# Performance work log

Hardware: AMD Instinct MI355X
Metric: run time of the kernel (lower is better)

## Reference

```python
import jax, jax.numpy as jnp
import numpy as np

B, E, F, H, C = 2048, 16, 512, 1024, 512
TOP_K = 4
TEMP = 1.0


def setup_inputs() -> dict:
    key = jax.random.key(0)
    ks = jax.random.split(key, 5)
    h = jax.random.normal(ks[0], (B, F), jnp.float32)
    # Router posterior params (xavier-ish mu, logvar init at -7 as in torch code)
    W_mu = jax.random.normal(ks[1], (E, F), jnp.float32) * (1.0 / np.sqrt(F))
    W_logvar = jnp.full((E, F), -7.0, jnp.float32)
    b_mu = jnp.zeros((E,), jnp.float32)
    b_logvar = jnp.full((E,), -7.0, jnp.float32)
    # Expert MLP params: layer1 [F->H] relu, layer2 [H->C]
    W1 = jax.random.normal(ks[2], (E, F, H), jnp.float32) * (1.0 / np.sqrt(F))
    b1 = jnp.zeros((E, H), jnp.float32)
    W2 = jax.random.normal(ks[3], (E, H, C), jnp.float32) * (1.0 / np.sqrt(H))
    b2 = jnp.zeros((E, C), jnp.float32)
    return {"h": h, "W_mu": W_mu, "b_mu": b_mu, "W_logvar": W_logvar,
            "b_logvar": b_logvar, "W1": W1, "b1": b1, "W2": W2, "b2": b2}


def reference(h, W_mu, b_mu, W_logvar, b_logvar, W1, b1, W2, b2):
    # Bayesian router moments: mu = h @ W_mu^T + b_mu ; var = (h*h) @ exp(W_logvar)^T + exp(b_logvar)
    mu_m = h @ W_mu.T + b_mu                                   # [B,E]
    var_m = (h * h) @ jnp.exp(W_logvar).T + jnp.exp(b_logvar)  # [B,E]
    var_m = jnp.maximum(var_m, 1e-12)
    # Logistic-normal shrink: tilde = mu / sqrt(1 + (pi/8) var)
    tilde_m = mu_m / jnp.sqrt(1.0 + (jnp.pi / 8.0) * var_m)
    gate_probs = jax.nn.softmax(tilde_m / TEMP, axis=-1)       # [B,E]
    # Strict top-k by gate_scores (tilde_m), renormalize probs within top-k
    topk_scores, topk_idx = jax.lax.top_k(tilde_m, TOP_K)      # [B,k]
    topk_w = jnp.take_along_axis(gate_probs, topk_idx, axis=1) # [B,k]
    topk_w = topk_w / jnp.maximum(topk_w.sum(axis=1, keepdims=True), 1e-12)
    # Dense combine weights: w[b,e] = sum of renormalized top-k weights of token b for expert e
    Bsz = h.shape[0]
    w = jnp.zeros((Bsz, E), h.dtype).at[jnp.arange(Bsz)[:, None], topk_idx].add(topk_w)
    # Expert MLPs (grouped GEMM form); tokens not routed to expert e get weight 0
    a = jax.nn.relu(jnp.einsum('bf,efh->beh', h, W1) + b1)     # [B,E,H]
    y = jnp.einsum('beh,ehc->bec', a, W2) + b2                 # [B,E,C]
    combined = jnp.einsum('be,bec->bc', w, y)                  # [B,C]
    return combined
```

## Files before the change

kernel.cpp:

```cpp
#include <hip/hip_runtime.h>
#include <hip/hip_bf16.h>

typedef __attribute__((ext_vector_type(8))) short bf16x8;
typedef __attribute__((ext_vector_type(4))) float f32x4;

#define NTOK   2048
#define NEXP   16
#define NF     512
#define NH     1024
#define NCOUT  512
#define NPAIR  8192

__device__ __forceinline__ void gload16_lds(const __hip_bfloat16* g, const __hip_bfloat16* l) {
  __builtin_amdgcn_global_load_lds((const __attribute__((address_space(1))) void*)g,
                                   (__attribute__((address_space(3))) void*)l, 16, 0, 0);
}

__global__ __launch_bounds__(256) void router_kernel(
    const float* __restrict__ h, const float* __restrict__ W_mu,
    const float* __restrict__ b_mu, const float* __restrict__ W_logvar,
    const float* __restrict__ b_logvar,
    int* __restrict__ topk_idx, float* __restrict__ topk_w,
    __hip_bfloat16* __restrict__ hb)
{
  __shared__ __align__(16) float hs[NF], hs2[NF];
  __shared__ float smu[NEXP], svar[NEXP];
  const int b = blockIdx.x, tid = threadIdx.x;
  for (int i = tid; i < NF; i += 256) {
    float v = h[(size_t)b * NF + i];
    hs[i] = v; hs2[i] = v * v;
    hb[(size_t)b * NF + i] = __float2bfloat16(v);
  }
  __syncthreads();
  const int e = tid >> 4, l = tid & 15;
  float mu = 0.f, var = 0.f;
  const float4* wm4 = (const float4*)(W_mu + e * NF);
  const float4* wv4 = (const float4*)(W_logvar + e * NF);
  const float4* h4  = (const float4*)hs;
  const float4* h24 = (const float4*)hs2;
#pragma unroll
  for (int j = 0; j < NF / 64; ++j) {
    int i4 = l + j * 16;
    float4 a = h4[i4],  wa = wm4[i4];
    float4 c = h24[i4], wc = wv4[i4];
    mu  += a.x * wa.x + a.y * wa.y + a.z * wa.z + a.w * wa.w;
    var += c.x * __expf(wc.x) + c.y * __expf(wc.y) + c.z * __expf(wc.z) + c.w * __expf(wc.w);
  }
#pragma unroll
  for (int o = 1; o < 16; o <<= 1) { mu += __shfl_xor(mu, o); var += __shfl_xor(var, o); }
  if (l == 0) { smu[e] = mu + b_mu[e]; svar[e] = var + __expf(b_logvar[e]); }
  __syncthreads();
  if (tid < 64) {
    float val = -1e30f;
    if (tid < NEXP) {
      float v = fmaxf(svar[tid], 1e-12f);
      val = smu[tid] / sqrtf(1.0f + 0.39269908169872414f * v);
    }
    float mx = 0.f, wsum = 0.f;
    int i0, i1, i2, i3; float p0, p1, p2, p3;
#define TOPK_ROUND(ii, pp, FIRST)                                          \
    {                                                                      \
      float m = val;                                                       \
      m = fmaxf(m, __shfl_xor(m, 1));  m = fmaxf(m, __shfl_xor(m, 2));     \
      m = fmaxf(m, __shfl_xor(m, 4));  m = fmaxf(m, __shfl_xor(m, 8));     \
      m = fmaxf(m, __shfl_xor(m, 16)); m = fmaxf(m, __shfl_xor(m, 32));    \
      unsigned long long bm = __ballot(val == m);                          \
      int bi = (int)__builtin_ctzll(bm);                                   \
      if (FIRST) mx = m;                                                   \
      pp = expf(m - mx); wsum += pp; ii = bi;                              \
      if (tid == bi) val = -1e30f;                                         \
    }
    TOPK_ROUND(i0, p0, 1)
    TOPK_ROUND(i1, p1, 0)
    TOPK_ROUND(i2, p2, 0)
    TOPK_ROUND(i3, p3, 0)
#undef TOPK_ROUND
    if (tid == 0) {
      float inv = 1.0f / fmaxf(wsum, 1e-12f);
      topk_idx[b * 4 + 0] = i0; topk_w[b * 4 + 0] = p0 * inv;
      topk_idx[b * 4 + 1] = i1; topk_w[b * 4 + 1] = p1 * inv;
      topk_idx[b * 4 + 2] = i2; topk_w[b * 4 + 2] = p2 * inv;
      topk_idx[b * 4 + 3] = i3; topk_w[b * 4 + 3] = p3 * inv;
    }
  }
}

__global__ __launch_bounds__(1024) void route_finish_kernel(
    const int* __restrict__ topk_idx,
    int* __restrict__ counts, int* __restrict__ offsets,
    int* __restrict__ token_of_row, int* __restrict__ pair_row)
{
  __shared__ int cnt[128][16];
  __shared__ int choff[128][2];
  __shared__ int tot[16];
  __shared__ int soff[16];
  const int tid = threadIdx.x;
  const int wv = tid >> 6, ln = tid & 63;
  const int e0 = blockIdx.x * 2;
  int mye[8], myrank[8];
#pragma unroll
  for (int r = 0; r < 8; ++r) {
    const int chunk = r * 16 + wv;
    const int t = chunk * 64 + ln;
    const int e = topk_idx[t];
    mye[r] = e;
    unsigned long long mymask = 0;
#pragma unroll
    for (int ee = 0; ee < 16; ++ee) {
      unsigned long long bmask = __ballot(e == ee);
      if (ln == 0) cnt[chunk][ee] = __popcll(bmask);
      if (e == ee) mymask = bmask;
    }
    myrank[r] = __popcll(mymask & ((1ull << ln) - 1ull));
  }
  __syncthreads();
  if (tid < 16) {
    int run = 0;
    for (int c = 0; c < 128; ++c) run += cnt[c][tid];
    tot[tid] = run;
    if (blockIdx.x == 0) counts[tid] = run;
  }
  if (tid >= 32 && tid < 34) {
    const int e = e0 + (tid - 32);
    int run = 0;
    for (int c = 0; c < 128; ++c) { choff[c][tid - 32] = run; run += cnt[c][e]; }
  }
  __syncthreads();
  if (tid == 0) {
    int run = 0;
    for (int e2 = 0; e2 < NEXP; ++e2) {
      soff[e2] = run;
      if (blockIdx.x == 0) offsets[e2] = run;
      run += tot[e2];
    }
  }
  __syncthreads();
#pragma unroll
  for (int r = 0; r < 8; ++r) {
    const int e = mye[r];
    if (e == e0 || e == e0 + 1) {
      const int chunk = r * 16 + wv;
      const int t = chunk * 64 + ln;
      const int pos = soff[e] + choff[chunk][e - e0] + myrank[r];
      token_of_row[pos] = t >> 2;
      pair_row[t] = pos;
    }
  }
}

__global__ __launch_bounds__(256) void transpose_convert_kernel(
    const float* __restrict__ in, __hip_bfloat16* __restrict__ out, int R, int C)
{
  __shared__ float tile[64][33];
  const int e = blockIdx.z;
  const int r0 = blockIdx.y * 64, c0 = blockIdx.x * 32;
  const int x = threadIdx.x & 31, y = threadIdx.x >> 5;
  const float* ip = in + ((size_t)e * R + r0) * C + c0;
#pragma unroll
  for (int i = 0; i < 8; ++i) tile[y + 8 * i][x] = ip[(size_t)(y + 8 * i) * C + x];
  __syncthreads();
  const int rp = threadIdx.x & 31, cb = threadIdx.x >> 5;
#pragma unroll
  for (int j = 0; j < 4; ++j) {
    const int c = cb + 8 * j;
    union { __hip_bfloat16 b[2]; unsigned u; } v;
    v.b[0] = __float2bfloat16(tile[2 * rp][c]);
    v.b[1] = __float2bfloat16(tile[2 * rp + 1][c]);
    *(unsigned*)(out + ((size_t)e * C + c0 + c) * R + r0 + 2 * rp) = v.u;
  }
}


__global__ __launch_bounds__(256) void gemm1_kernel(
    const __hip_bfloat16* __restrict__ hb,
    const __hip_bfloat16* __restrict__ W1t,
    const float* __restrict__ b1,
    const int* __restrict__ token_of_row, const int* __restrict__ offsets,
    const int* __restrict__ counts,
    __hip_bfloat16* __restrict__ a_out)
{
  const int bid = blockIdx.x;
  const int id  = (bid & 7) * 512 + (bid >> 3);
  const int e   = id >> 8;
  const int m0  = ((id >> 4) & 15) * 128;
  const int n0  = (id & 15) * 64;
  const int cnt = counts[e];
  if (m0 >= cnt) return;
  const int off = offsets[e];

  __shared__ __align__(16) __hip_bfloat16 As[128 * 64];
  __shared__ __align__(16) __hip_bfloat16 Bs[64 * 64];

  const int tid = threadIdx.x;
  const int w = tid >> 6, l = tid & 63;
  const int wm = w >> 1, wn = w & 1;
  const int r16 = l & 15, g4 = l >> 4;
  const int sx = r16 & 7;
  const int koffL = (((l & 7) ^ (l >> 3)) * 8);

  const __hip_bfloat16* Aptr[4];
#pragma unroll
  for (int i = 0; i < 4; ++i) {
    int r = off + m0 + w * 32 + i * 8 + (l >> 3);
    if (r > NPAIR - 1) r = NPAIR - 1;
    Aptr[i] = hb + (size_t)token_of_row[r] * NF + koffL;
  }
  const __hip_bfloat16* Bptr[2];
#pragma unroll
  for (int i = 0; i < 2; ++i)
    Bptr[i] = W1t + ((size_t)e * NH + n0 + w * 16 + i * 8 + (l >> 3)) * NF + koffL;

  f32x4 acc[4][2] = {};

  for (int k0 = 0; k0 < NF; k0 += 64) {
    __syncthreads();
#pragma unroll
    for (int i = 0; i < 4; ++i) gload16_lds(Aptr[i] + k0, As + (w * 32 + i * 8) * 64);
#pragma unroll
    for (int i = 0; i < 2; ++i) gload16_lds(Bptr[i] + k0, Bs + (w * 16 + i * 8) * 64);
    __syncthreads();
#pragma unroll
    for (int ks = 0; ks < 2; ++ks) {
      const int seg = (ks * 4 + g4) ^ sx;
      bf16x8 af[4], bq[2];
#pragma unroll
      for (int rr = 0; rr < 4; ++rr)
        af[rr] = *(const bf16x8*)(As + (wm * 64 + rr * 16 + r16) * 64 + seg * 8);
#pragma unroll
      for (int nn = 0; nn < 2; ++nn)
        bq[nn] = *(const bf16x8*)(Bs + (wn * 32 + nn * 16 + r16) * 64 + seg * 8);
#pragma unroll
      for (int rr = 0; rr < 4; ++rr)
#pragma unroll
        for (int nn = 0; nn < 2; ++nn)
          acc[rr][nn] = __builtin_amdgcn_mfma_f32_16x16x32_bf16(af[rr], bq[nn], acc[rr][nn], 0, 0, 0);
    }
  }

  const int q4 = l >> 4, cl = l & 15;
  const int mmax = cnt - m0;
#pragma unroll
  for (int rr = 0; rr < 4; ++rr) {
#pragma unroll
    for (int nn = 0; nn < 2; ++nn) {
      const int c = n0 + wn * 32 + nn * 16 + cl;
      const float bias = b1[e * NH + c];
#pragma unroll
      for (int q = 0; q < 4; ++q) {
        const int r = wm * 64 + rr * 16 + q4 * 4 + q;
        if (r < mmax) {
          float v = fmaxf(acc[rr][nn][q] + bias, 0.f);
          a_out[(size_t)(off + m0 + r) * NH + c] = __float2bfloat16(v);
        }
      }
    }
  }
}

__global__ __launch_bounds__(256) void gemm2_kernel(
    const __hip_bfloat16* __restrict__ a_in,
    const __hip_bfloat16* __restrict__ W2t,
    const float* __restrict__ b2,
    const int* __restrict__ offsets, const int* __restrict__ counts,
    float* __restrict__ ybuf)
{
  const int bid = blockIdx.x;
  const int id  = (bid & 7) * 256 + (bid >> 3);
  const int e   = id >> 7;
  const int m0  = ((id >> 3) & 15) * 128;
  const int n0  = (id & 7) * 64;
  const int cnt = counts[e];
  if (m0 >= cnt) return;
  const int off = offsets[e];

  __shared__ __align__(16) __hip_bfloat16 As[128 * 64];
  __shared__ __align__(16) __hip_bfloat16 Bs[64 * 64];

  const int tid = threadIdx.x;
  const int w = tid >> 6, l = tid & 63;
  const int wm = w >> 1, wn = w & 1;
  const int r16 = l & 15, g4 = l >> 4;
  const int sx = r16 & 7;
  const int koffL = (((l & 7) ^ (l >> 3)) * 8);

  const __hip_bfloat16* Aptr[4];
#pragma unroll
  for (int i = 0; i < 4; ++i) {
    int r = off + m0 + w * 32 + i * 8 + (l >> 3);
    if (r > NPAIR - 1) r = NPAIR - 1;
    Aptr[i] = a_in + (size_t)r * NH + koffL;
  }
  const __hip_bfloat16* Bptr[2];
#pragma unroll
  for (int i = 0; i < 2; ++i)
    Bptr[i] = W2t + ((size_t)e * NCOUT + n0 + w * 16 + i * 8 + (l >> 3)) * NH + koffL;

  f32x4 acc[4][2] = {};

  for (int k0 = 0; k0 < NH; k0 += 64) {
    __syncthreads();
#pragma unroll
    for (int i = 0; i < 4; ++i) gload16_lds(Aptr[i] + k0, As + (w * 32 + i * 8) * 64);
#pragma unroll
    for (int i = 0; i < 2; ++i) gload16_lds(Bptr[i] + k0, Bs + (w * 16 + i * 8) * 64);
    __syncthreads();
#pragma unroll
    for (int ks = 0; ks < 2; ++ks) {
      const int seg = (ks * 4 + g4) ^ sx;
      bf16x8 af[4], bq[2];
#pragma unroll
      for (int rr = 0; rr < 4; ++rr)
        af[rr] = *(const bf16x8*)(As + (wm * 64 + rr * 16 + r16) * 64 + seg * 8);
#pragma unroll
      for (int nn = 0; nn < 2; ++nn)
        bq[nn] = *(const bf16x8*)(Bs + (wn * 32 + nn * 16 + r16) * 64 + seg * 8);
#pragma unroll
      for (int rr = 0; rr < 4; ++rr)
#pragma unroll
        for (int nn = 0; nn < 2; ++nn)
          acc[rr][nn] = __builtin_amdgcn_mfma_f32_16x16x32_bf16(af[rr], bq[nn], acc[rr][nn], 0, 0, 0);
    }
  }

  const int q4 = l >> 4, cl = l & 15;
  const int mmax = cnt - m0;
#pragma unroll
  for (int rr = 0; rr < 4; ++rr) {
#pragma unroll
    for (int nn = 0; nn < 2; ++nn) {
      const int c = n0 + wn * 32 + nn * 16 + cl;
      const float bias = b2[e * NCOUT + c];
#pragma unroll
      for (int q = 0; q < 4; ++q) {
        const int r = wm * 64 + rr * 16 + q4 * 4 + q;
        if (r < mmax)
          ybuf[(size_t)(off + m0 + r) * NCOUT + c] = acc[rr][nn][q] + bias;
      }
    }
  }
}

__global__ __launch_bounds__(256) void combine_kernel(
    const float* __restrict__ ybuf, const int* __restrict__ pair_row,
    const float* __restrict__ topk_w, float* __restrict__ out)
{
  const int tok = blockIdx.x;
  const int c = threadIdx.x * 2;
  float a0 = 0.f, a1 = 0.f;
#pragma unroll
  for (int k = 0; k < 4; ++k) {
    const int t = tok * 4 + k;
    const float wt = topk_w[t];
    const float2 y = *(const float2*)(ybuf + (size_t)pair_row[t] * NCOUT + c);
    a0 += wt * y.x; a1 += wt * y.y;
  }
  *(float2*)(out + (size_t)tok * NCOUT + c) = make_float2(a0, a1);
}

extern "C" void kernel_launch(void* const* d_in, const int* in_sizes, int n_in,
                              void* d_out, int out_size, void* d_ws, size_t ws_size,
                              hipStream_t stream) {
  (void)in_sizes; (void)n_in; (void)ws_size; (void)out_size;
  const float* h        = (const float*)d_in[0];
  const float* W_mu     = (const float*)d_in[1];
  const float* b_mu     = (const float*)d_in[2];
  const float* W_logvar = (const float*)d_in[3];
  const float* b_logvar = (const float*)d_in[4];
  const float* W1       = (const float*)d_in[5];
  const float* b1       = (const float*)d_in[6];
  const float* W2       = (const float*)d_in[7];
  const float* b2       = (const float*)d_in[8];
  float* out = (float*)d_out;

  char* p = (char*)d_ws;
  int*   counts   = (int*)p;   p += 16 * 4;
  int*   offsets  = (int*)p;   p += 16 * 4;
  p += 32 * 4;
  int*   topk_idx = (int*)p;   p += (size_t)NPAIR * 4;
  float* topk_w   = (float*)p; p += (size_t)NPAIR * 4;
  int*   tok_row  = (int*)p;   p += (size_t)NPAIR * 4;
  int*   pair_row = (int*)p;   p += (size_t)NPAIR * 4;
  __hip_bfloat16* hb   = (__hip_bfloat16*)p; p += (size_t)NTOK * NF * 2;
  __hip_bfloat16* W1t  = (__hip_bfloat16*)p; p += (size_t)NEXP * NF * NH * 2;
  __hip_bfloat16* W2t  = (__hip_bfloat16*)p; p += (size_t)NEXP * NH * NCOUT * 2;
  __hip_bfloat16* abuf = (__hip_bfloat16*)p; p += (size_t)NPAIR * NH * 2;
  float*          ybuf = (float*)p;          p += (size_t)NPAIR * NCOUT * 4;

  router_kernel<<<NTOK, 256, 0, stream>>>(h, W_mu, b_mu, W_logvar, b_logvar,
                                          topk_idx, topk_w, hb);
  route_finish_kernel<<<8, 1024, 0, stream>>>(topk_idx, counts, offsets, tok_row, pair_row);

  transpose_convert_kernel<<<dim3(NH / 32, NF / 64, NEXP), 256, 0, stream>>>(W1, W1t, NF, NH);
  transpose_convert_kernel<<<dim3(NCOUT / 32, NH / 64, NEXP), 256, 0, stream>>>(W2, W2t, NH, NCOUT);

  gemm1_kernel<<<4096, 256, 0, stream>>>(hb, W1t, b1, tok_row, offsets, counts, abuf);
  gemm2_kernel<<<2048, 256, 0, stream>>>(abuf, W2t, b2, offsets, counts, ybuf);
  combine_kernel<<<NTOK, 256, 0, stream>>>(ybuf, pair_row, topk_w, out);
}
```

Before: 92.87 us.

## Split-K gemm2 into two halves and merge weight transpose launches

The second expert GEMM is split along K into two halves. Each half writes partial sums to its own y buffer, with the bias added only on the first half, and the combine kernel sums the two partials. This doubles the number of blocks so more CUs are busy when per-expert row counts are uneven. It costs twice the ybuf writes and reads plus an extra 16MB of workspace. The two W1/W2 transpose-convert launches are also fused into a single launch to remove one kernel launch overhead.

```diff
diff --git a/kernel.cpp b/kernel.cpp
--- a/kernel.cpp
+++ b/kernel.cpp
@@ -149,11 +149,21 @@
 }
 
 __global__ __launch_bounds__(256) void transpose_convert_kernel(
-    const float* __restrict__ in, __hip_bfloat16* __restrict__ out, int R, int C)
-{
+    const float* __restrict__ W1, __hip_bfloat16* __restrict__ W1t,
+    const float* __restrict__ W2, __hip_bfloat16* __restrict__ W2t)
+{
+  const int bid = blockIdx.x;
+  const float* in; __hip_bfloat16* out; int R, C, e, cx, ry;
+  if (bid < 4096) {
+    in = W1; out = W1t; R = NF; C = NH;
+    e = bid >> 8; cx = bid & 31; ry = (bid >> 5) & 7;
+  } else {
+    in = W2; out = W2t; R = NH; C = NCOUT;
+    const int b2 = bid - 4096;
+    e = b2 >> 8; cx = b2 & 15; ry = (b2 >> 4) & 15;
+  }
   __shared__ float tile[64][33];
-  const int e = blockIdx.z;
-  const int r0 = blockIdx.y * 64, c0 = blockIdx.x * 32;
+  const int r0 = ry * 64, c0 = cx * 32;
   const int x = threadIdx.x & 31, y = threadIdx.x >> 5;
   const float* ip = in + ((size_t)e * R + r0) * C + c0;
 #pragma unroll
@@ -265,13 +275,16 @@
     float* __restrict__ ybuf)
 {
   const int bid = blockIdx.x;
-  const int id  = (bid & 7) * 256 + (bid >> 3);
-  const int e   = id >> 7;
-  const int m0  = ((id >> 3) & 15) * 128;
+  const int id  = (bid & 7) * 512 + (bid >> 3);
+  const int e   = id >> 8;
+  const int m0  = ((id >> 4) & 15) * 128;
+  const int kc  = (id >> 3) & 1;
   const int n0  = (id & 7) * 64;
   const int cnt = counts[e];
   if (m0 >= cnt) return;
   const int off = offsets[e];
+  const int koff = kc * (NH / 2);
+  float* yout = ybuf + (size_t)kc * NPAIR * NCOUT;
 
   __shared__ __align__(16) __hip_bfloat16 As[128 * 64];
   __shared__ __align__(16) __hip_bfloat16 Bs[64 * 64];
@@ -288,16 +301,16 @@
   for (int i = 0; i < 4; ++i) {
     int r = off + m0 + w * 32 + i * 8 + (l >> 3);
     if (r > NPAIR - 1) r = NPAIR - 1;
-    Aptr[i] = a_in + (size_t)r * NH + koffL;
+    Aptr[i] = a_in + (size_t)r * NH + koff + koffL;
   }
   const __hip_bfloat16* Bptr[2];
 #pragma unroll
   for (int i = 0; i < 2; ++i)
-    Bptr[i] = W2t + ((size_t)e * NCOUT + n0 + w * 16 + i * 8 + (l >> 3)) * NH + koffL;
+    Bptr[i] = W2t + ((size_t)e * NCOUT + n0 + w * 16 + i * 8 + (l >> 3)) * NH + koff + koffL;
 
   f32x4 acc[4][2] = {};
 
-  for (int k0 = 0; k0 < NH; k0 += 64) {
+  for (int k0 = 0; k0 < NH / 2; k0 += 64) {
     __syncthreads();
 #pragma unroll
     for (int i = 0; i < 4; ++i) gload16_lds(Aptr[i] + k0, As + (w * 32 + i * 8) * 64);
@@ -329,12 +342,12 @@
 #pragma unroll
     for (int nn = 0; nn < 2; ++nn) {
       const int c = n0 + wn * 32 + nn * 16 + cl;
-      const float bias = b2[e * NCOUT + c];
+      const float bias = (kc == 0) ? b2[e * NCOUT + c] : 0.f;
 #pragma unroll
       for (int q = 0; q < 4; ++q) {
         const int r = wm * 64 + rr * 16 + q4 * 4 + q;
         if (r < mmax)
-          ybuf[(size_t)(off + m0 + r) * NCOUT + c] = acc[rr][nn][q] + bias;
+          yout[(size_t)(off + m0 + r) * NCOUT + c] = acc[rr][nn][q] + bias;
       }
     }
   }
@@ -351,8 +364,10 @@
   for (int k = 0; k < 4; ++k) {
     const int t = tok * 4 + k;
     const float wt = topk_w[t];
-    const float2 y = *(const float2*)(ybuf + (size_t)pair_row[t] * NCOUT + c);
-    a0 += wt * y.x; a1 += wt * y.y;
+    const size_t base = (size_t)pair_row[t] * NCOUT + c;
+    const float2 y0 = *(const float2*)(ybuf + base);
+    const float2 y1 = *(const float2*)(ybuf + (size_t)NPAIR * NCOUT + base);
+    a0 += wt * (y0.x + y1.x); a1 += wt * (y0.y + y1.y);
   }
   *(float2*)(out + (size_t)tok * NCOUT + c) = make_float2(a0, a1);
 }
@@ -384,16 +399,15 @@
   __hip_bfloat16* W1t  = (__hip_bfloat16*)p; p += (size_t)NEXP * NF * NH * 2;
   __hip_bfloat16* W2t  = (__hip_bfloat16*)p; p += (size_t)NEXP * NH * NCOUT * 2;
   __hip_bfloat16* abuf = (__hip_bfloat16*)p; p += (size_t)NPAIR * NH * 2;
-  float*          ybuf = (float*)p;          p += (size_t)NPAIR * NCOUT * 4;
+  float*          ybuf = (float*)p;          p += (size_t)2 * NPAIR * NCOUT * 4;
 
   router_kernel<<<NTOK, 256, 0, stream>>>(h, W_mu, b_mu, W_logvar, b_logvar,
                                           topk_idx, topk_w, hb);
   route_finish_kernel<<<8, 1024, 0, stream>>>(topk_idx, counts, offsets, tok_row, pair_row);
 
-  transpose_convert_kernel<<<dim3(NH / 32, NF / 64, NEXP), 256, 0, stream>>>(W1, W1t, NF, NH);
-  transpose_convert_kernel<<<dim3(NCOUT / 32, NH / 64, NEXP), 256, 0, stream>>>(W2, W2t, NH, NCOUT);
+  transpose_convert_kernel<<<8192, 256, 0, stream>>>(W1, W1t, W2, W2t);
 
   gemm1_kernel<<<4096, 256, 0, stream>>>(hb, W1t, b1, tok_row, offsets, counts, abuf);
-  gemm2_kernel<<<2048, 256, 0, stream>>>(abuf, W2t, b2, offsets, counts, ybuf);
+  gemm2_kernel<<<4096, 256, 0, stream>>>(abuf, W2t, b2, offsets, counts, ybuf);
   combine_kernel<<<NTOK, 256, 0, stream>>>(ybuf, pair_row, topk_w, out);
 }
```

After: 92.67 us. About the same (-0.2%).

## Double-buffer LDS staging in expert GEMMs and merge weight transpose launches

Applied to the files above, without the earlier changes.

Both grouped GEMM kernels now keep two LDS buffers and issue the global-to-LDS loads for the next K tile before computing on the current one. They wait with vmcnt(6) so the load latency overlaps the MFMA work. Separately, the two weight transpose/convert launches become one 8192-block launch that picks W1 or W2 from the block index, saving a launch. Doubling LDS per block (48KB) may lower occupancy.

```diff
diff --git a/kernel.cpp b/kernel.cpp
--- a/kernel.cpp
+++ b/kernel.cpp
@@ -149,11 +149,21 @@
 }
 
 __global__ __launch_bounds__(256) void transpose_convert_kernel(
-    const float* __restrict__ in, __hip_bfloat16* __restrict__ out, int R, int C)
-{
+    const float* __restrict__ W1, __hip_bfloat16* __restrict__ W1t,
+    const float* __restrict__ W2, __hip_bfloat16* __restrict__ W2t)
+{
+  const int bid = blockIdx.x;
+  const float* in; __hip_bfloat16* out; int R, C, e, cx, ry;
+  if (bid < 4096) {
+    in = W1; out = W1t; R = NF; C = NH;
+    e = bid >> 8; cx = bid & 31; ry = (bid >> 5) & 7;
+  } else {
+    in = W2; out = W2t; R = NH; C = NCOUT;
+    const int b2 = bid - 4096;
+    e = b2 >> 8; cx = b2 & 15; ry = (b2 >> 4) & 15;
+  }
   __shared__ float tile[64][33];
-  const int e = blockIdx.z;
-  const int r0 = blockIdx.y * 64, c0 = blockIdx.x * 32;
+  const int r0 = ry * 64, c0 = cx * 32;
   const int x = threadIdx.x & 31, y = threadIdx.x >> 5;
   const float* ip = in + ((size_t)e * R + r0) * C + c0;
 #pragma unroll
@@ -188,8 +198,8 @@
   if (m0 >= cnt) return;
   const int off = offsets[e];
 
-  __shared__ __align__(16) __hip_bfloat16 As[128 * 64];
-  __shared__ __align__(16) __hip_bfloat16 Bs[64 * 64];
+  __shared__ __align__(16) __hip_bfloat16 As[2][128 * 64];
+  __shared__ __align__(16) __hip_bfloat16 Bs[2][64 * 64];
 
   const int tid = threadIdx.x;
   const int w = tid >> 6, l = tid & 63;
@@ -210,32 +220,42 @@
   for (int i = 0; i < 2; ++i)
     Bptr[i] = W1t + ((size_t)e * NH + n0 + w * 16 + i * 8 + (l >> 3)) * NF + koffL;
 
+#define STG1(bf, k0) { \
+  _Pragma("unroll") for (int i = 0; i < 4; ++i) gload16_lds(Aptr[i] + (k0), &As[bf][(w * 32 + i * 8) * 64]); \
+  _Pragma("unroll") for (int i = 0; i < 2; ++i) gload16_lds(Bptr[i] + (k0), &Bs[bf][(w * 16 + i * 8) * 64]); }
+
   f32x4 acc[4][2] = {};
-
-  for (int k0 = 0; k0 < NF; k0 += 64) {
-    __syncthreads();
-#pragma unroll
-    for (int i = 0; i < 4; ++i) gload16_lds(Aptr[i] + k0, As + (w * 32 + i * 8) * 64);
-#pragma unroll
-    for (int i = 0; i < 2; ++i) gload16_lds(Bptr[i] + k0, Bs + (w * 16 + i * 8) * 64);
-    __syncthreads();
+  const int NT = NF / 64;
+
+  STG1(0, 0)
+  for (int t = 0; t < NT; ++t) {
+    const int cur = t & 1;
+    if (t + 1 < NT) {
+      STG1(cur ^ 1, (t + 1) * 64)
+      asm volatile("s_waitcnt vmcnt(6)" ::: "memory");
+    } else {
+      asm volatile("s_waitcnt vmcnt(0)" ::: "memory");
+    }
+    __builtin_amdgcn_s_barrier();
 #pragma unroll
     for (int ks = 0; ks < 2; ++ks) {
       const int seg = (ks * 4 + g4) ^ sx;
       bf16x8 af[4], bq[2];
 #pragma unroll
       for (int rr = 0; rr < 4; ++rr)
-        af[rr] = *(const bf16x8*)(As + (wm * 64 + rr * 16 + r16) * 64 + seg * 8);
+        af[rr] = *(const bf16x8*)(&As[cur][(wm * 64 + rr * 16 + r16) * 64 + seg * 8]);
 #pragma unroll
       for (int nn = 0; nn < 2; ++nn)
-        bq[nn] = *(const bf16x8*)(Bs + (wn * 32 + nn * 16 + r16) * 64 + seg * 8);
+        bq[nn] = *(const bf16x8*)(&Bs[cur][(wn * 32 + nn * 16 + r16) * 64 + seg * 8]);
 #pragma unroll
       for (int rr = 0; rr < 4; ++rr)
 #pragma unroll
         for (int nn = 0; nn < 2; ++nn)
           acc[rr][nn] = __builtin_amdgcn_mfma_f32_16x16x32_bf16(af[rr], bq[nn], acc[rr][nn], 0, 0, 0);
     }
-  }
+    if (t + 1 < NT) __builtin_amdgcn_s_barrier();
+  }
+#undef STG1
 
   const int q4 = l >> 4, cl = l & 15;
   const int mmax = cnt - m0;
@@ -273,8 +293,8 @@
   if (m0 >= cnt) return;
   const int off = offsets[e];
 
-  __shared__ __align__(16) __hip_bfloat16 As[128 * 64];
-  __shared__ __align__(16) __hip_bfloat16 Bs[64 * 64];
+  __shared__ __align__(16) __hip_bfloat16 As[2][128 * 64];
+  __shared__ __align__(16) __hip_bfloat16 Bs[2][64 * 64];
 
   const int tid = threadIdx.x;
   const int w = tid >> 6, l = tid & 63;
@@ -295,32 +315,42 @@
   for (int i = 0; i < 2; ++i)
     Bptr[i] = W2t + ((size_t)e * NCOUT + n0 + w * 16 + i * 8 + (l >> 3)) * NH + koffL;
 
+#define STG2(bf, k0) { \
+  _Pragma("unroll") for (int i = 0; i < 4; ++i) gload16_lds(Aptr[i] + (k0), &As[bf][(w * 32 + i * 8) * 64]); \
+  _Pragma("unroll") for (int i = 0; i < 2; ++i) gload16_lds(Bptr[i] + (k0), &Bs[bf][(w * 16 + i * 8) * 64]); }
+
   f32x4 acc[4][2] = {};
-
-  for (int k0 = 0; k0 < NH; k0 += 64) {
-    __syncthreads();
-#pragma unroll
-    for (int i = 0; i < 4; ++i) gload16_lds(Aptr[i] + k0, As + (w * 32 + i * 8) * 64);
-#pragma unroll
-    for (int i = 0; i < 2; ++i) gload16_lds(Bptr[i] + k0, Bs + (w * 16 + i * 8) * 64);
-    __syncthreads();
+  const int NT = NH / 64;
+
+  STG2(0, 0)
+  for (int t = 0; t < NT; ++t) {
+    const int cur = t & 1;
+    if (t + 1 < NT) {
+      STG2(cur ^ 1, (t + 1) * 64)
+      asm volatile("s_waitcnt vmcnt(6)" ::: "memory");
+    } else {
+      asm volatile("s_waitcnt vmcnt(0)" ::: "memory");
+    }
+    __builtin_amdgcn_s_barrier();
 #pragma unroll
     for (int ks = 0; ks < 2; ++ks) {
       const int seg = (ks * 4 + g4) ^ sx;
       bf16x8 af[4], bq[2];
 #pragma unroll
       for (int rr = 0; rr < 4; ++rr)
-        af[rr] = *(const bf16x8*)(As + (wm * 64 + rr * 16 + r16) * 64 + seg * 8);
+        af[rr] = *(const bf16x8*)(&As[cur][(wm * 64 + rr * 16 + r16) * 64 + seg * 8]);
 #pragma unroll
       for (int nn = 0; nn < 2; ++nn)
-        bq[nn] = *(const bf16x8*)(Bs + (wn * 32 + nn * 16 + r16) * 64 + seg * 8);
+        bq[nn] = *(const bf16x8*)(&Bs[cur][(wn * 32 + nn * 16 + r16) * 64 + seg * 8]);
 #pragma unroll
       for (int rr = 0; rr < 4; ++rr)
 #pragma unroll
         for (int nn = 0; nn < 2; ++nn)
           acc[rr][nn] = __builtin_amdgcn_mfma_f32_16x16x32_bf16(af[rr], bq[nn], acc[rr][nn], 0, 0, 0);
     }
-  }
+    if (t + 1 < NT) __builtin_amdgcn_s_barrier();
+  }
+#undef STG2
 
   const int q4 = l >> 4, cl = l & 15;
   const int mmax = cnt - m0;
@@ -390,8 +420,7 @@
                                           topk_idx, topk_w, hb);
   route_finish_kernel<<<8, 1024, 0, stream>>>(topk_idx, counts, offsets, tok_row, pair_row);
 
-  transpose_convert_kernel<<<dim3(NH / 32, NF / 64, NEXP), 256, 0, stream>>>(W1, W1t, NF, NH);
-  transpose_convert_kernel<<<dim3(NCOUT / 32, NH / 64, NEXP), 256, 0, stream>>>(W2, W2t, NH, NCOUT);
+  transpose_convert_kernel<<<8192, 256, 0, stream>>>(W1, W1t, W2, W2t);
 
   gemm1_kernel<<<4096, 256, 0, stream>>>(hb, W1t, b1, tok_row, offsets, counts, abuf);
   gemm2_kernel<<<2048, 256, 0, stream>>>(abuf, W2t, b2, offsets, counts, ybuf);
```

After: 92.75 us. About the same (-0.1%).
